# Kernel tuning notes

Hardware: AMD Instinct MI355X
Metric: run time of the kernel (lower is better)

Reference implementation:

```python
import jax, jax.numpy as jnp
import numpy as np

N, D = 8192, 256

def _gram_rbf(x, y, sigma):
    x2 = jnp.sum(x * x, axis=-1)                      # [N]
    y2 = jnp.sum(y * y, axis=-1)                      # [M]
    xy = jnp.einsum('nd,md->nm', x, y)                # [N,M] GEMM
    sq = x2[:, None] + y2[None, :] - 2.0 * xy
    return jnp.exp(-sq / sigma)

def setup_inputs() -> dict:
    key = jax.random.key(0)
    k1, k2 = jax.random.split(key)
    return {
        'input': jax.random.normal(k1, (N, D), dtype=jnp.float32),
        'target': jax.random.normal(k2, (N, D), dtype=jnp.float32) + 0.5,
        'sigma': 256,
    }

def reference(input, target, sigma):
    XX = _gram_rbf(input, input, sigma)
    YY = _gram_rbf(target, target, sigma)
    XY = _gram_rbf(input, target, sigma)
    return jnp.mean(XX) + jnp.mean(YY) - 2.0 * jnp.mean(XY)
```

## Files before the change

### kernel.cpp

```cpp
#include <hip/hip_runtime.h>
#include <hip/hip_bf16.h>
#include <stdint.h>
#include <stddef.h>


#define N_PTS   8192
#define DIM     256
#define TWO_N   16384
#define CS2     16

#define AS1 __attribute__((address_space(1)))
#define AS3 __attribute__((address_space(3)))

typedef __attribute__((ext_vector_type(4))) float f32x4;
typedef __attribute__((ext_vector_type(4))) int   i32x4;
typedef __attribute__((ext_vector_type(8))) int   i32x8;

__global__ __launch_bounds__(256) void mmd_prep(const float* __restrict__ X,
                                                const float* __restrict__ Y,
                                                const int* __restrict__ sigmap,
                                                unsigned char* __restrict__ Zf8,
                                                float* __restrict__ n2,
                                                float* __restrict__ out) {
    if (blockIdx.x == 0 && threadIdx.x == 0) out[0] = 0.0f;

    const int wave = threadIdx.x >> 6;
    const int lane = threadIdx.x & 63;
    const int row  = blockIdx.x * 4 + wave;

    const float* src = (row < N_PTS) ? (X + (size_t)row * DIM)
                                     : (Y + (size_t)(row - N_PTS) * DIM);
    float4 v = ((const float4*)src)[lane];

    float s = v.x * v.x + v.y * v.y + v.z * v.z + v.w * v.w;
#pragma unroll
    for (int off = 32; off; off >>= 1) s += __shfl_down(s, off, 64);
    if (lane == 0) {
        const float c2 = -1.4426950408889634f / (float)(*sigmap);
        n2[row] = c2 * s;
    }

    const int p01 = __builtin_amdgcn_cvt_pk_fp8_f32(v.x, v.y, 0, false);
    const int p23 = __builtin_amdgcn_cvt_pk_fp8_f32(v.z, v.w, 0, false);
    const unsigned int pk = ((unsigned)p01 & 0xffffu) | ((unsigned)p23 << 16);
    *(unsigned int*)(Zf8 + (size_t)row * DIM + (size_t)lane * 4) = pk;
}

__global__ __launch_bounds__(256, 3) void mmd_main(const unsigned char* __restrict__ Zf8,
                                                   const float* __restrict__ n2,
                                                   const int* __restrict__ sigmap,
                                                   float* __restrict__ out) {
    __shared__ char smem_b[32768];
    __shared__ float n2rS[128];
    __shared__ float wsum[4];

    const int bid = (int)blockIdx.x;
    const int br  = 127 - (bid >> 4);
    const int cs  = bid & (CS2 - 1);
    const int bcMax = 2 * br + 1;
    if (cs > bcMax) return;

    const int t    = threadIdx.x;
    const int wave = t >> 6;
    const int lane = t & 63;
    const int wm   = wave >> 1;
    const int wn   = wave & 1;
    const int g    = lane >> 4;
    const int ml   = lane & 15;
    const int rowBase = br * 128;

    const float m2 = 2.8853900817779268f / (float)(*sigmap);
    const int   SC = 0x7f7f7f7f;

    {
        const int colBase0 = cs * 64;
#pragma unroll
        for (int i = 0; i < 4; ++i) {
            const int cidx = i * 256 + t;
            const int col  = cidx >> 4;
            const int s    = cidx & 15;
            const int gc   = s ^ (col & 15);
            const unsigned char* gp = Zf8 + (size_t)(colBase0 + col) * DIM + gc * 16;
            __builtin_amdgcn_global_load_lds((const AS1 void*)gp,
                                             (AS3 void*)(smem_b + (size_t)cidx * 16), 16, 0, 0);
        }
    }
    if (t < 128) n2rS[t] = n2[rowBase + t];

    i32x8 af[4][2];
#pragma unroll
    for (int mt = 0; mt < 4; ++mt) {
        const unsigned char* rp =
            Zf8 + (size_t)(rowBase + wm * 64 + mt * 16 + ml) * DIM + g * 32;
#pragma unroll
        for (int kc = 0; kc < 2; ++kc) {
            union { i32x4 h[2]; i32x8 v; } u;
            u.h[0] = *(const i32x4*)(rp + kc * 128);
            u.h[1] = *(const i32x4*)(rp + kc * 128 + 16);
            af[mt][kc] = u.v;
        }
    }

    float block_acc = 0.0f;
    const int brX = (br < 64);
    int cur = 0;

    for (int bc = cs; bc <= bcMax; bc += CS2) {
        const int colBase = bc * 64;

        float b_j[2];
#pragma unroll
        for (int nt = 0; nt < 2; ++nt)
            b_j[nt] = n2[colBase + wn * 32 + nt * 16 + ml];

        f32x4 acc[4][2] = {};

        __syncthreads();

        if (bc + CS2 <= bcMax) {
            const int colBaseN = colBase + CS2 * 64;
            char* dst = smem_b + (cur ^ 1) * 16384;
#pragma unroll
            for (int i = 0; i < 4; ++i) {
                const int cidx = i * 256 + t;
                const int col  = cidx >> 4;
                const int s    = cidx & 15;
                const int gc   = s ^ (col & 15);
                const unsigned char* gp = Zf8 + (size_t)(colBaseN + col) * DIM + gc * 16;
                __builtin_amdgcn_global_load_lds((const AS1 void*)gp,
                                                 (AS3 void*)(dst + (size_t)cidx * 16), 16, 0, 0);
            }
        }

        const char* buf = smem_b + cur * 16384;
#pragma unroll
        for (int kc = 0; kc < 2; ++kc) {
            const int j0 = kc * 8 + g * 2;
            i32x8 bf[2];
#pragma unroll
            for (int nt = 0; nt < 2; ++nt) {
                const int col = wn * 32 + nt * 16 + ml;
                const char* cb = buf + (size_t)col * 256;
                union { i32x4 h[2]; i32x8 v; } u;
                u.h[0] = *(const i32x4*)(cb + (size_t)((j0)     ^ (col & 15)) * 16);
                u.h[1] = *(const i32x4*)(cb + (size_t)((j0 + 1) ^ (col & 15)) * 16);
                bf[nt] = u.v;
            }
#pragma unroll
            for (int mt = 0; mt < 4; ++mt)
#pragma unroll
                for (int nt = 0; nt < 2; ++nt)
                    acc[mt][nt] = __builtin_amdgcn_mfma_scale_f32_16x16x128_f8f6f4(
                        af[mt][kc], bf[nt], acc[mt][nt],
                        0, 0,
                        0, SC,
                        0, SC);
        }

        float ts0 = 0.0f, ts1 = 0.0f, ts2 = 0.0f, ts3 = 0.0f;
#pragma unroll
        for (int mt = 0; mt < 4; ++mt) {
            const f32x4 ar = *(const f32x4*)&n2rS[wm * 64 + mt * 16 + g * 4];
#pragma unroll
            for (int nt = 0; nt < 2; ++nt) {
                const float ab = b_j[nt];
                ts0 += __builtin_amdgcn_exp2f(fmaf(acc[mt][nt][0], m2, ar[0] + ab));
                ts1 += __builtin_amdgcn_exp2f(fmaf(acc[mt][nt][1], m2, ar[1] + ab));
                ts2 += __builtin_amdgcn_exp2f(fmaf(acc[mt][nt][2], m2, ar[2] + ab));
                ts3 += __builtin_amdgcn_exp2f(fmaf(acc[mt][nt][3], m2, ar[3] + ab));
            }
        }
        const float tsum = (ts0 + ts1) + (ts2 + ts3);

        const float sgn = ((bc < 128) == brX) ? 1.0f : -1.0f;
        const float w   = (bc < 2 * br) ? 2.0f * sgn : sgn;
        block_acc = fmaf(w, tsum, block_acc);
        cur ^= 1;
    }

    float s = block_acc;
#pragma unroll
    for (int off = 32; off; off >>= 1) s += __shfl_down(s, off, 64);
    if (lane == 0) wsum[wave] = s;
    __syncthreads();
    if (t == 0)
        atomicAdd(out, (wsum[0] + wsum[1] + wsum[2] + wsum[3]) * (1.0f / 67108864.0f));
}

extern "C" void kernel_launch(void* const* d_in, const int* in_sizes, int n_in,
                              void* d_out, int out_size, void* d_ws, size_t ws_size,
                              hipStream_t stream) {
    const float* X      = (const float*)d_in[0];
    const float* Y      = (const float*)d_in[1];
    const int*   sigmap = (const int*)d_in[2];
    float*       out    = (float*)d_out;

    unsigned char* Zf8 = (unsigned char*)d_ws;
    float*         n2  = (float*)((char*)d_ws + (size_t)TWO_N * DIM);

    mmd_prep<<<TWO_N / 4, 256, 0, stream>>>(X, Y, sigmap, Zf8, n2, out);
    mmd_main<<<128 * CS2, 256, 0, stream>>>(Zf8, n2, sigmap, out);
}
```

Before: 122.9 us.

## Software-pipeline MFMA compute with previous tile's exp epilogue using ping-pong accumulators

Splits the loop so the MFMA accumulation for the current column tile runs alongside the exp2 epilogue of the previous tile, using two accumulator sets that alternate. The aim is to hide transcendental-unit latency behind matrix-core work. It also precomputes the global and LDS swizzle offsets once outside the loop. The extra accumulators raise register pressure, so launch bounds drop from 3 to 2 blocks per SIMD, which lowers occupancy.

```diff
diff --git a/kernel.cpp b/kernel.cpp
--- a/kernel.cpp
+++ b/kernel.cpp
@@ -46,7 +46,7 @@
     *(unsigned int*)(Zf8 + (size_t)row * DIM + (size_t)lane * 4) = pk;
 }
 
-__global__ __launch_bounds__(256, 3) void mmd_main(const unsigned char* __restrict__ Zf8,
+__global__ __launch_bounds__(256, 2) void mmd_main(const unsigned char* __restrict__ Zf8,
                                                    const float* __restrict__ n2,
                                                    const int* __restrict__ sigmap,
                                                    float* __restrict__ out) {
@@ -68,22 +68,40 @@
     const int g    = lane >> 4;
     const int ml   = lane & 15;
     const int rowBase = br * 128;
+    const int brX  = (br < 64);
 
     const float m2 = 2.8853900817779268f / (float)(*sigmap);
     const int   SC = 0x7f7f7f7f;
 
+    int g_off[4], l_off[4];
+#pragma unroll
+    for (int i = 0; i < 4; ++i) {
+        const int cidx = i * 256 + t;
+        const int col  = cidx >> 4;
+        const int s    = cidx & 15;
+        const int gc   = s ^ (col & 15);
+        g_off[i] = col * DIM + gc * 16;
+        l_off[i] = cidx * 16;
+    }
+
+    int bfo[2][2][2];
+#pragma unroll
+    for (int kc = 0; kc < 2; ++kc) {
+        const int j0 = kc * 8 + g * 2;
+#pragma unroll
+        for (int nt = 0; nt < 2; ++nt) {
+            const int col = wn * 32 + nt * 16 + ml;
+            bfo[kc][nt][0] = col * 256 + ((j0)     ^ (col & 15)) * 16;
+            bfo[kc][nt][1] = col * 256 + ((j0 + 1) ^ (col & 15)) * 16;
+        }
+    }
+
     {
-        const int colBase0 = cs * 64;
-#pragma unroll
-        for (int i = 0; i < 4; ++i) {
-            const int cidx = i * 256 + t;
-            const int col  = cidx >> 4;
-            const int s    = cidx & 15;
-            const int gc   = s ^ (col & 15);
-            const unsigned char* gp = Zf8 + (size_t)(colBase0 + col) * DIM + gc * 16;
-            __builtin_amdgcn_global_load_lds((const AS1 void*)gp,
-                                             (AS3 void*)(smem_b + (size_t)cidx * 16), 16, 0, 0);
-        }
+        const unsigned char* base = Zf8 + (size_t)(cs * 64) * DIM;
+#pragma unroll
+        for (int i = 0; i < 4; ++i)
+            __builtin_amdgcn_global_load_lds((const AS1 void*)(base + g_off[i]),
+                                             (AS3 void*)(smem_b + l_off[i]), 16, 0, 0);
     }
     if (t < 128) n2rS[t] = n2[rowBase + t];
 
@@ -101,82 +119,103 @@
         }
     }
 
+    f32x4 accA[4][2], accB[4][2];
     float block_acc = 0.0f;
-    const int brX = (br < 64);
-    int cur = 0;
-
-    for (int bc = cs; bc <= bcMax; bc += CS2) {
-        const int colBase = bc * 64;
-
-        float b_j[2];
-#pragma unroll
-        for (int nt = 0; nt < 2; ++nt)
-            b_j[nt] = n2[colBase + wn * 32 + nt * 16 + ml];
-
-        f32x4 acc[4][2] = {};
+
+#define ZERO_ACC(ACC)                                                         \
+    {                                                                         \
+        _Pragma("unroll") for (int mt = 0; mt < 4; ++mt)                      \
+            _Pragma("unroll") for (int nt = 0; nt < 2; ++nt)                  \
+                ACC[mt][nt] = (f32x4){0.f, 0.f, 0.f, 0.f};                    \
+    }
+
+#define COMPUTE(ACC, BUFR)                                                    \
+    {                                                                         \
+        _Pragma("unroll") for (int kc = 0; kc < 2; ++kc) {                    \
+            i32x8 bf[2];                                                      \
+            _Pragma("unroll") for (int nt = 0; nt < 2; ++nt) {                \
+                union { i32x4 h[2]; i32x8 v; } u;                             \
+                u.h[0] = *(const i32x4*)((BUFR) + bfo[kc][nt][0]);            \
+                u.h[1] = *(const i32x4*)((BUFR) + bfo[kc][nt][1]);            \
+                bf[nt] = u.v;                                                 \
+            }                                                                 \
+            _Pragma("unroll") for (int mt = 0; mt < 4; ++mt)                  \
+                _Pragma("unroll") for (int nt = 0; nt < 2; ++nt)              \
+                    ACC[mt][nt] = __builtin_amdgcn_mfma_scale_f32_16x16x128_f8f6f4( \
+                        af[mt][kc], bf[nt], ACC[mt][nt], 0, 0, 0, SC, 0, SC); \
+        }                                                                     \
+    }
+
+#define EPILOGUE(ACC, B0, B1, W)                                              \
+    {                                                                         \
+        float t0 = 0.f, t1 = 0.f, t2 = 0.f, t3 = 0.f;                         \
+        _Pragma("unroll") for (int mt = 0; mt < 4; ++mt) {                    \
+            const f32x4 ar = *(const f32x4*)&n2rS[wm * 64 + mt * 16 + g * 4]; \
+            {                                                                 \
+                t0 += __builtin_amdgcn_exp2f(fmaf(ACC[mt][0][0], m2, ar[0] + (B0))); \
+                t1 += __builtin_amdgcn_exp2f(fmaf(ACC[mt][0][1], m2, ar[1] + (B0))); \
+                t2 += __builtin_amdgcn_exp2f(fmaf(ACC[mt][0][2], m2, ar[2] + (B0))); \
+                t3 += __builtin_amdgcn_exp2f(fmaf(ACC[mt][0][3], m2, ar[3] + (B0))); \
+                t0 += __builtin_amdgcn_exp2f(fmaf(ACC[mt][1][0], m2, ar[0] + (B1))); \
+                t1 += __builtin_amdgcn_exp2f(fmaf(ACC[mt][1][1], m2, ar[1] + (B1))); \
+                t2 += __builtin_amdgcn_exp2f(fmaf(ACC[mt][1][2], m2, ar[2] + (B1))); \
+                t3 += __builtin_amdgcn_exp2f(fmaf(ACC[mt][1][3], m2, ar[3] + (B1))); \
+            }                                                                 \
+        }                                                                     \
+        block_acc = fmaf((W), (t0 + t1) + (t2 + t3), block_acc);              \
+    }
+
+#define WEIGHT(BC) ((((BC) < 128) == brX ? 1.0f : -1.0f) * ((BC) < 2 * br ? 2.0f : 1.0f))
+
+    const char* bufR = smem_b;
+    char*       bufW = smem_b + 16384;
+
+    float pB0 = n2[cs * 64 + wn * 32 + ml];
+    float pB1 = n2[cs * 64 + wn * 32 + 16 + ml];
+    float pW  = WEIGHT(cs);
+
+    __syncthreads();
+    if (cs + CS2 <= bcMax) {
+        const unsigned char* base = Zf8 + (size_t)((cs + CS2) * 64) * DIM;
+#pragma unroll
+        for (int i = 0; i < 4; ++i)
+            __builtin_amdgcn_global_load_lds((const AS1 void*)(base + g_off[i]),
+                                             (AS3 void*)(bufW + l_off[i]), 16, 0, 0);
+    }
+    ZERO_ACC(accA);
+    COMPUTE(accA, bufR);
+
+    bool pendA = true;
+    for (int bc = cs + CS2; bc <= bcMax; bc += CS2) {
+        const float cB0 = n2[bc * 64 + wn * 32 + ml];
+        const float cB1 = n2[bc * 64 + wn * 32 + 16 + ml];
+
+        { const char* tmp = bufR; bufR = bufW; bufW = (char*)tmp; }
 
         __syncthreads();
-
         if (bc + CS2 <= bcMax) {
-            const int colBaseN = colBase + CS2 * 64;
-            char* dst = smem_b + (cur ^ 1) * 16384;
-#pragma unroll
-            for (int i = 0; i < 4; ++i) {
-                const int cidx = i * 256 + t;
-                const int col  = cidx >> 4;
-                const int s    = cidx & 15;
-                const int gc   = s ^ (col & 15);
-                const unsigned char* gp = Zf8 + (size_t)(colBaseN + col) * DIM + gc * 16;
-                __builtin_amdgcn_global_load_lds((const AS1 void*)gp,
-                                                 (AS3 void*)(dst + (size_t)cidx * 16), 16, 0, 0);
-            }
-        }
-
-        const char* buf = smem_b + cur * 16384;
-#pragma unroll
-        for (int kc = 0; kc < 2; ++kc) {
-            const int j0 = kc * 8 + g * 2;
-            i32x8 bf[2];
-#pragma unroll
-            for (int nt = 0; nt < 2; ++nt) {
-                const int col = wn * 32 + nt * 16 + ml;
-                const char* cb = buf + (size_t)col * 256;
-                union { i32x4 h[2]; i32x8 v; } u;
-                u.h[0] = *(const i32x4*)(cb + (size_t)((j0)     ^ (col & 15)) * 16);
-                u.h[1] = *(const i32x4*)(cb + (size_t)((j0 + 1) ^ (col & 15)) * 16);
-                bf[nt] = u.v;
-            }
-#pragma unroll
-            for (int mt = 0; mt < 4; ++mt)
-#pragma unroll
-                for (int nt = 0; nt < 2; ++nt)
-                    acc[mt][nt] = __builtin_amdgcn_mfma_scale_f32_16x16x128_f8f6f4(
-                        af[mt][kc], bf[nt], acc[mt][nt],
-                        0, 0,
-                        0, SC,
-                        0, SC);
-        }
-
-        float ts0 = 0.0f, ts1 = 0.0f, ts2 = 0.0f, ts3 = 0.0f;
-#pragma unroll
-        for (int mt = 0; mt < 4; ++mt) {
-            const f32x4 ar = *(const f32x4*)&n2rS[wm * 64 + mt * 16 + g * 4];
-#pragma unroll
-            for (int nt = 0; nt < 2; ++nt) {
-                const float ab = b_j[nt];
-                ts0 += __builtin_amdgcn_exp2f(fmaf(acc[mt][nt][0], m2, ar[0] + ab));
-                ts1 += __builtin_amdgcn_exp2f(fmaf(acc[mt][nt][1], m2, ar[1] + ab));
-                ts2 += __builtin_amdgcn_exp2f(fmaf(acc[mt][nt][2], m2, ar[2] + ab));
-                ts3 += __builtin_amdgcn_exp2f(fmaf(acc[mt][nt][3], m2, ar[3] + ab));
-            }
-        }
-        const float tsum = (ts0 + ts1) + (ts2 + ts3);
-
-        const float sgn = ((bc < 128) == brX) ? 1.0f : -1.0f;
-        const float w   = (bc < 2 * br) ? 2.0f * sgn : sgn;
-        block_acc = fmaf(w, tsum, block_acc);
-        cur ^= 1;
-    }
+            const unsigned char* base = Zf8 + (size_t)((bc + CS2) * 64) * DIM;
+#pragma unroll
+            for (int i = 0; i < 4; ++i)
+                __builtin_amdgcn_global_load_lds((const AS1 void*)(base + g_off[i]),
+                                                 (AS3 void*)(bufW + l_off[i]), 16, 0, 0);
+        }
+
+        if (pendA) {
+            ZERO_ACC(accB);
+            COMPUTE(accB, bufR);
+            EPILOGUE(accA, pB0, pB1, pW);
+        } else {
+            ZERO_ACC(accA);
+            COMPUTE(accA, bufR);
+            EPILOGUE(accB, pB0, pB1, pW);
+        }
+        pendA = !pendA;
+        pB0 = cB0; pB1 = cB1; pW = WEIGHT(bc);
+    }
+
+    if (pendA) { EPILOGUE(accA, pB0, pB1, pW); }
+    else       { EPILOGUE(accB, pB0, pB1, pW); }
 
     float s = block_acc;
 #pragma unroll
```

New measurement: 154.3 us. 25.6% more time.
